# Kernel optimization log

Hardware: AMD Instinct MI355X
Metric: run time of the kernel (lower is better)

The kernel has to match this reference:

```python
import jax, jax.numpy as jnp
import numpy as np

U10_IDX, V10_IDX = 0, 1
WIND_THRESH = 0.5


def _gru(x, h, Wih, Whh, bih, bhh):
    # standard torch GRUCell math
    gi = x @ Wih.T + bih
    gh = h @ Whh.T + bhh
    ir, iz, inn = jnp.split(gi, 3, axis=-1)
    hr, hz, hnn = jnp.split(gh, 3, axis=-1)
    r = jax.nn.sigmoid(ir + hr)
    z = jax.nn.sigmoid(iz + hz)
    n = jnp.tanh(inn + r * hnn)
    return (1.0 - z) * n + z * h


def setup_inputs() -> dict:
    B, N, H, F, Th, Tf = 256, 184, 128, 8, 24, 24
    key = jax.random.key(0)
    ks = jax.random.split(key, 24)
    s = 0.1
    f32 = jnp.float32
    feature = jax.random.normal(ks[0], (B, Th + Tf, N, F), f32)
    pm25_hist = jax.random.uniform(ks[1], (B, Th, N, 1), dtype=f32)
    adj_mat = (jax.random.uniform(ks[2], (N, N)) < 0.1).astype(f32)
    angles = jax.random.uniform(ks[3], (N, N), f32, 0.0, 2.0 * np.pi)
    C = F + 1  # ChebConv in-channels = in_dim + out_dim
    return dict(
        feature=feature, pm25_hist=pm25_hist, adj_mat=adj_mat, angles=angles,
        W_ih_hist=s * jax.random.normal(ks[4], (3 * H, 2), f32),
        W_hh_hist=s * jax.random.normal(ks[5], (3 * H, H), f32),
        b_ih_hist=s * jax.random.normal(ks[6], (3 * H,), f32),
        b_hh_hist=s * jax.random.normal(ks[7], (3 * H,), f32),
        fc_hist_w=s * jax.random.normal(ks[8], (1, H), f32),
        fc_hist_b=s * jax.random.normal(ks[9], (1,), f32),
        cheb_w0=s * jax.random.normal(ks[10], (C, 1), f32),
        cheb_w1=s * jax.random.normal(ks[11], (C, 1), f32),
        cheb_b=s * jax.random.normal(ks[12], (1,), f32),
        W_ih=s * jax.random.normal(ks[13], (3 * H, C + 1), f32),
        W_hh=s * jax.random.normal(ks[14], (3 * H, H), f32),
        b_ih=s * jax.random.normal(ks[15], (3 * H,), f32),
        b_hh=s * jax.random.normal(ks[16], (3 * H,), f32),
        fc_out_w=s * jax.random.normal(ks[17], (1, H), f32),
        fc_out_b=s * jax.random.normal(ks[18], (1,), f32),
    )


def reference(feature, pm25_hist, adj_mat, angles,
              W_ih_hist, W_hh_hist, b_ih_hist, b_hh_hist,
              fc_hist_w, fc_hist_b,
              cheb_w0, cheb_w1, cheb_b,
              W_ih, W_hh, b_ih, b_hh,
              fc_out_w, fc_out_b):
    B, T, N, F = feature.shape
    H = W_hh.shape[1]
    Th = pm25_hist.shape[1]
    comp1 = jnp.cos(angles)                                # [N,N]
    comp2 = jnp.cos(angles - jnp.float32(np.pi / 2.0))     # [N,N]
    adj_b = adj_mat > 0

    # ---- history GRU over pm25_hist ----
    def hist_step(carry, p):
        hn, xn = carry
        x = jnp.concatenate([xn, p], axis=-1).reshape(B * N, 2)
        hn = _gru(x, hn, W_ih_hist, W_hh_hist, b_ih_hist, b_hh_hist)
        xn = hn.reshape(B, N, H) @ fc_hist_w.T + fc_hist_b
        return (hn, xn), None

    h0 = jnp.zeros((B * N, H), feature.dtype)
    x0 = jnp.zeros((B, N, 1), feature.dtype)
    (hn, xn), _ = jax.lax.scan(hist_step, (h0, x0), jnp.swapaxes(pm25_hist, 0, 1))

    # ---- forecast: dynamic wind-gated graph + ChebConv(K=2) + GRU ----
    def fore_step(carry, f):
        hn, xn = carry
        x = jnp.concatenate([xn, f], axis=-1)              # [B,N,F+1]
        u = f[..., U10_IDX]                                # [B,N]
        v = f[..., V10_IDX]
        wind = u[:, :, None] * comp1[None] + v[:, :, None] * comp2[None]
        # edge i->j iff adj and wind projection >= threshold
        M = jnp.logical_and(wind >= WIND_THRESH, adj_b[None]).astype(x.dtype)
        deg = M.sum(-1)                                    # source degree [B,N]
        has = deg > 0
        dinv = jnp.where(has, 1.0 / jnp.sqrt(jnp.where(has, deg, 1.0)), 0.0)
        # ChebConv scaled Laplacian (lambda_max=2, sym norm):
        # L_hat x [j] = -dinv_j * sum_i dinv_i * M[i,j] * x[i] + (0 if deg_j>0 else -1) * x[j]
        y = jnp.einsum('bij,bic->bjc', M * dinv[:, :, None], x)
        y = -dinv[:, :, None] * y + jnp.where(has, 0.0, -1.0)[:, :, None] * x
        g = jax.nn.sigmoid(x @ cheb_w0 + y @ cheb_w1 + cheb_b)  # [B,N,1]
        x2 = jnp.concatenate([x, g], axis=-1).reshape(B * N, F + 2)
        hn = _gru(x2, hn, W_ih, W_hh, b_ih, b_hh)
        xn = hn.reshape(B, N, H) @ fc_out_w.T + fc_out_b
        return (hn, xn), xn

    fore_feat = jnp.swapaxes(feature[:, Th:], 0, 1)        # [Tf,B,N,F]
    (_, _), preds = jax.lax.scan(fore_step, (hn, xn), fore_feat)
    return jnp.swapaxes(preds, 0, 1)                       # [B,Tf,N,1]
```

## Files before the change

### kernel.cpp

```cpp
#include <hip/hip_runtime.h>
#include <hip/hip_bf16.h>
#include <math.h>

#define BB 256
#define NN 184
#define HH 128
#define FF 8
#define TH 24
#define TF 24
#define KA 160
#define NG2 640
#define RPAD 192
#define STRH 136
#define NT 1024
#define NW3 552
#define LOG2E 1.44269504088896f

#define REC_F 8832
#define OFF_DINV 4416
#define OFF_G 5152
#define OFF_AXF 5888

typedef __attribute__((ext_vector_type(8))) short bf16x8;
typedef __attribute__((ext_vector_type(4))) short bf16x4;
typedef __attribute__((ext_vector_type(4))) float f32x4;
typedef __attribute__((ext_vector_type(2))) unsigned u32x2;

#if __has_builtin(__builtin_amdgcn_mfma_f32_16x16x16bf16_1k)
#define XK16 1
#else
#define XK16 0
#endif

#if __has_builtin(__builtin_amdgcn_exp2f)
#define EXP2(x) __builtin_amdgcn_exp2f(x)
#else
#define EXP2(x) exp2f(x)
#endif

__device__ __forceinline__ unsigned short f2bf(float f) {
    unsigned u = __float_as_uint(f);
    u += 0x7fffu + ((u >> 16) & 1u);
    return (unsigned short)(u >> 16);
}
__device__ __forceinline__ unsigned pkbf(float a, float b) {
    __hip_bfloat162 h = __float22bfloat162_rn(make_float2(a, b));
    return *reinterpret_cast<unsigned*>(&h);
}
__device__ __forceinline__ void gload16(const void* src, void* dst) {
    __builtin_amdgcn_global_load_lds(
        (const __attribute__((address_space(1))) unsigned int*)src,
        (__attribute__((address_space(3))) unsigned int*)dst, 16, 0, 0);
}

__global__ void prep_weights(const float* __restrict__ WhhH, const float* __restrict__ WihH,
                             const float* __restrict__ WhhF, const float* __restrict__ WihF,
                             const float* __restrict__ bihH, const float* __restrict__ bhhH,
                             const float* __restrict__ bihF, const float* __restrict__ bhhF,
                             const float* __restrict__ fchw, const float* __restrict__ fchb,
                             unsigned short* __restrict__ WaH, unsigned short* __restrict__ WaF) {
    int idx = blockIdx.x * 256 + threadIdx.x;
    if (idx >= NG2 * KA) return;
    int jp = idx / KA, k = idx % KA;
    int j = jp & 127, part = jp >> 7;
    float vh = 0.f, vf = 0.f;
    if (part <= 1) {
        int row = part * 128 + j;
        if (k < 128) {
            vh = WhhH[row * 128 + k] + WihH[row * 2 + 0] * fchw[k];
            vf = WhhF[row * 128 + k];
        } else {
            int s = k - 128;
            if (s == 0)  vh = WihH[row * 2 + 1];
            if (s < 8)   vf = WihF[row * 10 + (s + 1)];
            if (s == 8)  { vh = WihH[row * 2 + 0]; vf = WihF[row * 10 + 0]; }
            if (s == 9)  vf = WihF[row * 10 + 9];
            if (s == 11) {
                vh = bihH[row] + bhhH[row] + WihH[row * 2 + 0] * fchb[0];
                vf = bihF[row] + bhhF[row];
            }
        }
    } else if (part == 2) {
        if (k < 128) { vh = WhhH[(256 + j) * 128 + k]; vf = WhhF[(256 + j) * 128 + k]; }
        else if (k == 139) { vh = bhhH[256 + j]; vf = bhhF[256 + j]; }
    } else if (part == 3) {
        if (k >= 128) {
            int s = k - 128;
            if (s == 0)  vh = WihH[(256 + j) * 2 + 1];
            if (s < 8)   vf = WihF[(256 + j) * 10 + (s + 1)];
            if (s == 8)  { vh = WihH[(256 + j) * 2 + 0]; vf = WihF[(256 + j) * 10 + 0]; }
            if (s == 9)  vf = WihF[(256 + j) * 10 + 9];
            if (s == 11) {
                vh = bihH[256 + j] + WihH[(256 + j) * 2 + 0] * fchb[0];
                vf = bihF[256 + j];
            }
        }
    } else {
        if (k < 128) vh = WihH[(256 + j) * 2 + 0] * fchw[k];
    }
    float sc = (part <= 1) ? LOG2E : 2.0f * LOG2E;
    WaH[idx] = f2bf(vh * sc);
    WaF[idx] = f2bf(vf * sc);
}

__global__ void prep_edges(const float* __restrict__ angles, const float* __restrict__ adj,
                           float4* __restrict__ edges, int* __restrict__ cnt) {
    int idx = blockIdx.x * 256 + threadIdx.x;
    if (idx < NN * NN && adj[idx] > 0.f) {
        float a = angles[idx];
        int pos = atomicAdd(cnt, 1);
        float4 r;
        r.x = cosf(a);
        r.y = cosf(a - 1.57079632679489662f);
        r.z = __int_as_float(idx / NN);
        r.w = __int_as_float(idx % NN);
        edges[pos] = r;
    }
}

__global__ __launch_bounds__(256) void prep_graph(
    const float* __restrict__ feature, const float* __restrict__ pm25,
    const float4* __restrict__ edges, const int* __restrict__ ecnt,
    const float* __restrict__ cw0, const float* __restrict__ cw1,
    const float* __restrict__ cbb, char* __restrict__ xrec,
    unsigned short* __restrict__ phist)
{
    const int bt = blockIdx.x;
    const int b = bt / (TH + TF), tt = bt % (TH + TF);
    const int tid = threadIdx.x;

    if (tt < TH) {
        if (tid < NN)
            phist[(long)b * (TH * NN) + tt * NN + tid] =
                f2bf(pm25[((long)b * TH + tt) * NN + tid]);
        return;
    }

    char* rec = xrec + ((long)b * TF + (tt - TH)) * REC_F;

    __shared__ float f8[NN * FF];
    __shared__ unsigned long long mT[NN][3];
    __shared__ int dg[NN];
    __shared__ float di[NN];
    __shared__ float red[NW3][8];

    const float4* fb4 = (const float4*)(feature + ((long)b * (TH + TF) + tt) * (NN * FF));
    for (int i = tid; i < (NN * FF) / 4; i += 256) ((float4*)f8)[i] = fb4[i];
    for (int i = tid; i < NN * 3; i += 256) ((unsigned long long*)mT)[i] = 0ull;
    for (int i = tid; i < NN; i += 256) dg[i] = 0;
    __syncthreads();
    const int nE = *ecnt;
    for (int e = tid; e < nE; e += 256) {
        float4 r = edges[e];
        int ii = __float_as_int(r.z), jj = __float_as_int(r.w);
        if (f8[ii * FF] * r.x + f8[ii * FF + 1] * r.y >= 0.5f) {
            atomicAdd(&dg[ii], 1);
            atomicOr(&mT[jj][ii >> 6], 1ull << (ii & 63));
        }
    }
    __syncthreads();
    if (tid < NN) di[tid] = (dg[tid] > 0) ? rsqrtf((float)dg[tid]) : 0.f;
    __syncthreads();
    unsigned long long* mr = (unsigned long long*)rec;
    for (int i = tid; i < NW3; i += 256) mr[i] = ((const unsigned long long*)mT)[i];
    for (int task = tid; task < NW3; task += 256) {
        int j = task / 3, wd = task - j * 3;
        unsigned long long m = mT[j][wd];
        float acc[8];
        #pragma unroll
        for (int c = 0; c < 8; ++c) acc[c] = 0.f;
        while (m) {
            int bp = __ffsll(m) - 1; m &= m - 1;
            int i = wd * 64 + bp;
            float d = di[i];
            #pragma unroll
            for (int c = 0; c < 8; ++c) acc[c] += d * f8[i * FF + c];
        }
        #pragma unroll
        for (int c = 0; c < 8; ++c) red[task][c] = acc[c];
    }
    __syncthreads();
    if (tid < NN) {
        int j = tid;
        float dj = di[j];
        float hzj = (dj > 0.f) ? 0.f : -1.f;
        float G = cbb[0];
        #pragma unroll
        for (int c = 0; c < 8; ++c) {
            float accc = red[j * 3 + 0][c] + red[j * 3 + 1][c] + red[j * 3 + 2][c];
            float xv = f8[j * FF + c];
            float y = -dj * accc + hzj * xv;
            G += xv * cw0[c + 1] + y * cw1[c + 1];
        }
        ((float*)(rec + OFF_DINV))[j] = dj;
        ((float*)(rec + OFF_G))[j] = G;
        unsigned short* ax = (unsigned short*)(rec + OFF_AXF) + j * 8;
        #pragma unroll
        for (int c = 0; c < 8; ++c) ax[c] = f2bf(f8[j * FF + c]);
    }
}

__global__ __launch_bounds__(NT, 4) void fused_dgc(
    const unsigned short* __restrict__ WaH,
    const unsigned short* __restrict__ WaF,
    const float* __restrict__ fchw, const float* __restrict__ fchb,
    const float* __restrict__ fcow, const float* __restrict__ fcob,
    const float* __restrict__ cw0, const float* __restrict__ cw1,
    const char* __restrict__ xrec, const unsigned short* __restrict__ phist,
    float* __restrict__ pred)
{
    __shared__ unsigned short Ah[2][RPAD * STRH];
    __shared__ unsigned short AxR[RPAD * 8];
    __shared__ __align__(16) char stg[2][8960];
    __shared__ float red_s[RPAD * 9];
    __shared__ float2 dx_s[NN];
    __shared__ float fcls_f[132];
    __shared__ unsigned short zero16[8];
    __shared__ __align__(16) unsigned short phist_s[TH * NN + 16];

    const int tid = threadIdx.x;
    const int bb = blockIdx.x;
    const int w = tid >> 6, lane = tid & 63, q = lane >> 4, lq = lane & 15;
    const int cg = w & 7, rh = w >> 3;

    for (int i = tid; i < RPAD * STRH; i += NT) Ah[0][i] = 0;
    for (int i = tid; i < RPAD * 8; i += NT)
        AxR[i] = ((i & 7) == 3) ? (unsigned short)0x3F80 : (unsigned short)0;
    if (tid < 8) zero16[tid] = 0;
    if (tid < NN) dx_s[tid] = make_float2(0.f, 0.f);

    bf16x8 wregH[4][4];
#if XK16
    bf16x4 wregX[4];
#else
    bf16x8 wregX[4];
#endif
    auto load_w = [&](const unsigned short* Wa, const float* fcw, const float* fcb, bool h4) {
        const int jcol = cg * 16 + lq;
        #pragma unroll
        for (int g = 0; g < 3; ++g)
            #pragma unroll
            for (int kc = 0; kc < 4; ++kc)
                wregH[g][kc] = *(const bf16x8*)(Wa + (long)(g * 128 + jcol) * KA + kc * 32 + q * 8);
        if (h4)
            #pragma unroll
            for (int kc = 0; kc < 4; ++kc)
                wregH[3][kc] = *(const bf16x8*)(Wa + (long)(4 * 128 + jcol) * KA + kc * 32 + q * 8);
        #pragma unroll
        for (int g = 0; g < 4; ++g)
#if XK16
            wregX[g] = *(const bf16x4*)(Wa + (long)(g * 128 + jcol) * KA + 128 + q * 4);
#else
            wregX[g] = *(const bf16x8*)(Wa + (long)(g * 128 + jcol) * KA + 128 + q * 8);
#endif
        if (tid < 132) fcls_f[tid] = (tid < 128) ? fcw[tid] : ((tid == 128) ? fcb[0] : 0.f);
    };
    load_w(WaH, fchw, fchb, true);

    if (tid < NW3)
        gload16((const char*)phist + (long)bb * (TH * NN * 2) + tid * 16,
                (char*)phist_s + (tid & ~63) * 16);

    const float w00 = cw0[0], w10 = cw1[0];
    const float fcbH = fchb[0];

    int p = 0;
    __syncthreads();

    for (int t = 0; t < TH + TF; ++t) {
        const bool hist = (t < TH);
        const bool dofc = (t >= TH - 1);
        const unsigned short* AxFS = (const unsigned short*)(stg[p] + OFF_AXF);

        if (!hist) {
            const unsigned long long* maskS = (const unsigned long long*)stg[p];
            const float* GS = (const float*)(stg[p] + OFF_G);
            const int jg = tid >> 2, wd = tid & 3;
            if (jg < NN) {
                unsigned long long m = (wd < 3) ? maskS[jg * 3 + wd] : 0ull;
                float acc = 0.f;
                while (m) {
                    int bp = __ffsll(m) - 1; m &= m - 1;
                    float2 dxv = dx_s[wd * 64 + bp];
                    acc += dxv.x * dxv.y;
                }
                acc += __shfl_xor(acc, 1);
                acc += __shfl_xor(acc, 2);
                if (wd == 0) {
                    float2 dxj = dx_s[jg];
                    float hzj = (dxj.x > 0.f) ? 0.f : -1.f;
                    float y0 = -dxj.x * acc + hzj * dxj.y;
                    float pre = GS[jg] + dxj.y * w00 + y0 * w10;
                    float g = __builtin_amdgcn_rcpf(1.0f + EXP2(-LOG2E * pre));
                    AxR[jg * 8 + 1] = f2bf(g);
                }
            }
            __syncthreads();
        }

        const int t2 = t + 1;
        if (t2 >= TH && t2 < TH + TF && tid < NW3)
            gload16(xrec + ((long)bb * TF + (t2 - TH)) * REC_F + tid * 16,
                    (char*)stg[p ^ 1] + (tid & ~63) * 16);

        f32x4 fw = *(const f32x4*)&fcls_f[cg * 16 + q * 4];
        const unsigned short corr0 = (t == 0) ? f2bf(-fcbH) : (unsigned short)0;
        #pragma unroll
        for (int rl = 0; rl < 6; ++rl) {
            const int row = rh * 96 + rl * 16 + lq;
            const int ro = row * STRH;
            f32x4 a0 = {0.f,0.f,0.f,0.f}, a1 = {0.f,0.f,0.f,0.f}, a2 = {0.f,0.f,0.f,0.f};
            f32x4 a3 = {0.f,0.f,0.f,0.f};
            #pragma unroll
            for (int kc = 0; kc < 4; ++kc) {
                bf16x8 bh = *(const bf16x8*)(&Ah[p][ro + kc * 32 + q * 8]);
                a0 = __builtin_amdgcn_mfma_f32_16x16x32_bf16(wregH[0][kc], bh, a0, 0, 0, 0);
                a1 = __builtin_amdgcn_mfma_f32_16x16x32_bf16(wregH[1][kc], bh, a1, 0, 0, 0);
                a2 = __builtin_amdgcn_mfma_f32_16x16x32_bf16(wregH[2][kc], bh, a2, 0, 0, 0);
                if (hist)
                    a3 = __builtin_amdgcn_mfma_f32_16x16x32_bf16(wregH[3][kc], bh, a3, 0, 0, 0);
            }
#if XK16
            bf16x4 bx;
            if (hist) {
                unsigned short pb = phist_s[t * NN + row];
                bf16x4 z = {0,0,0,0};
                bx = z;
                if (q == 0) bx[0] = (short)pb;
                if (q == 2) { bx[0] = (short)corr0; bx[3] = (short)0x3F80; }
            } else {
                const unsigned short* bxp = (q < 2) ? (AxFS + row * 8 + q * 4)
                                          : (q == 2) ? (AxR + row * 8) : zero16;
                bx = *(const bf16x4*)bxp;
            }
            a0 = __builtin_amdgcn_mfma_f32_16x16x16bf16_1k(wregX[0], bx, a0, 0, 0, 0);
            a1 = __builtin_amdgcn_mfma_f32_16x16x16bf16_1k(wregX[1], bx, a1, 0, 0, 0);
            a2 = __builtin_amdgcn_mfma_f32_16x16x16bf16_1k(wregX[2], bx, a2, 0, 0, 0);
            a3 = __builtin_amdgcn_mfma_f32_16x16x16bf16_1k(wregX[3], bx, a3, 0, 0, 0);
#else
            bf16x8 bx;
            if (hist) {
                unsigned short pb = phist_s[t * NN + row];
                bf16x8 z = {0,0,0,0,0,0,0,0};
                bx = z;
                if (q == 0) bx[0] = (short)pb;
                if (q == 1) { bx[0] = (short)corr0; bx[3] = (short)0x3F80; }
            } else {
                const unsigned short* bxp = (q == 0) ? (AxFS + row * 8)
                                          : (q == 1) ? (AxR + row * 8) : zero16;
                bx = *(const bf16x8*)bxp;
            }
            a0 = __builtin_amdgcn_mfma_f32_16x16x32_bf16(wregX[0], bx, a0, 0, 0, 0);
            a1 = __builtin_amdgcn_mfma_f32_16x16x32_bf16(wregX[1], bx, a1, 0, 0, 0);
            a2 = __builtin_amdgcn_mfma_f32_16x16x32_bf16(wregX[2], bx, a2, 0, 0, 0);
            a3 = __builtin_amdgcn_mfma_f32_16x16x32_bf16(wregX[3], bx, a3, 0, 0, 0);
#endif

            u32x2 hold = *(const u32x2*)&Ah[p][ro + cg * 16 + q * 4];

            float hn[4];
            #pragma unroll
            for (int rg = 0; rg < 4; ++rg) {
                unsigned hu = hold[rg >> 1];
                float ho = ((rg & 1) == 0) ? __uint_as_float(hu << 16)
                                           : __uint_as_float(hu & 0xffff0000u);
                float rr = __builtin_amdgcn_rcpf(1.0f + EXP2(-a0[rg]));
                float zz = __builtin_amdgcn_rcpf(1.0f + EXP2(-a1[rg]));
                float wv = fmaf(rr, a2[rg], a3[rg]);
                unsigned sg = __float_as_uint(wv) & 0x80000000u;
                float e = EXP2(-fabsf(wv));
                float tv = (1.0f - e) * __builtin_amdgcn_rcpf(1.0f + e);
                tv = __uint_as_float(__float_as_uint(tv) ^ sg);
                hn[rg] = fmaf(zz, ho - tv, tv);
            }
            u32x2 pk;
            pk[0] = pkbf(hn[0], hn[1]);
            pk[1] = pkbf(hn[2], hn[3]);
            *(u32x2*)&Ah[p ^ 1][ro + cg * 16 + q * 4] = pk;
            if (dofc) {
                float pf = hn[0] * fw.x + hn[1] * fw.y + hn[2] * fw.z + hn[3] * fw.w;
                pf += __shfl_xor(pf, 16);
                pf += __shfl_xor(pf, 32);
                if (q == 0) red_s[row * 9 + cg] = pf;
            }
        }
        __syncthreads();

        if (dofc) {
            if (tid < NN) {
                float xn = fcls_f[128];
                #pragma unroll
                for (int c = 0; c < 8; ++c) xn += red_s[tid * 9 + c];
                float dv = 0.f;
                if (t2 >= TH && t2 < TH + TF)
                    dv = *(const float*)(stg[p ^ 1] + OFF_DINV + tid * 4);
                dx_s[tid] = make_float2(dv, xn);
                AxR[tid * 8 + 0] = f2bf(xn);
                if (t >= TH) pred[((long)bb * TF + (t - TH)) * NN + tid] = xn;
            }
            __syncthreads();
        }

        if (t == TH - 1)
            load_w(WaF, fcow, fcob, false);
        p ^= 1;
    }
}

extern "C" void kernel_launch(void* const* d_in, const int* in_sizes, int n_in,
                              void* d_out, int out_size, void* d_ws, size_t ws_size,
                              hipStream_t stream) {
    const float* feature = (const float*)d_in[0];
    const float* pm25    = (const float*)d_in[1];
    const float* adj     = (const float*)d_in[2];
    const float* angles  = (const float*)d_in[3];
    const float* W_ih_h  = (const float*)d_in[4];
    const float* W_hh_h  = (const float*)d_in[5];
    const float* b_ih_h  = (const float*)d_in[6];
    const float* b_hh_h  = (const float*)d_in[7];
    const float* fch_w   = (const float*)d_in[8];
    const float* fch_b   = (const float*)d_in[9];
    const float* cw0     = (const float*)d_in[10];
    const float* cw1     = (const float*)d_in[11];
    const float* cbb     = (const float*)d_in[12];
    const float* W_ih    = (const float*)d_in[13];
    const float* W_hh    = (const float*)d_in[14];
    const float* b_ih    = (const float*)d_in[15];
    const float* b_hh    = (const float*)d_in[16];
    const float* fco_w   = (const float*)d_in[17];
    const float* fco_b   = (const float*)d_in[18];
    float* pred = (float*)d_out;

    char* ws = (char*)d_ws;
    size_t off = 0;
    unsigned short* WaH   = (unsigned short*)(ws + off); off += (size_t)NG2 * KA * 2;
    unsigned short* WaF   = (unsigned short*)(ws + off); off += (size_t)NG2 * KA * 2;
    float4*         edges = (float4*)(ws + off);         off += (size_t)NN * NN * 16;
    int*            cnt   = (int*)(ws + off);            off += 16;
    unsigned short* phist = (unsigned short*)(ws + off); off += (size_t)BB * TH * NN * 2;
    char*           xrec  = (char*)(ws + off);
    off += (size_t)BB * TF * REC_F;

    hipMemsetAsync(cnt, 0, 16, stream);
    prep_weights<<<(NG2 * KA + 255) / 256, 256, 0, stream>>>(
        W_hh_h, W_ih_h, W_hh, W_ih, b_ih_h, b_hh_h, b_ih, b_hh, fch_w, fch_b,
        WaH, WaF);
    prep_edges<<<(NN * NN + 255) / 256, 256, 0, stream>>>(angles, adj, edges, cnt);
    prep_graph<<<BB * (TH + TF), 256, 0, stream>>>(
        feature, pm25, edges, cnt, cw0, cw1, cbb, xrec, phist);

    fused_dgc<<<BB, NT, 0, stream>>>(
        WaH, WaF, fch_w, fch_b, fco_w, fco_b, cw0, cw1, xrec, phist, pred);
}
```

Baseline: 645.0 us.

## Fold fc-output reduction into graph step via shared atomics, drop extra barrier

The per-row fc output is now accumulated with shared-memory atomics into a double-buffered xnraw array instead of a red_s buffer followed by a separate reduction pass and barrier. The bias add, the bf16 write into AxR, the prediction store and the dinv lookup move into the next step's graph-convolution phase, which removes one __syncthreads per timestep. The history pm25 conversion is split into its own small elementwise kernel, so prep_graph launches only forecast blocks. Shared atomics add contention (8 adds per row), and the bias for the first forecast step is handled as a special case.

```diff
diff --git a/kernel.cpp b/kernel.cpp
--- a/kernel.cpp
+++ b/kernel.cpp
@@ -118,25 +118,23 @@
     }
 }
 
+__global__ void prep_hist(const float* __restrict__ pm25, unsigned short* __restrict__ phist) {
+    int idx = blockIdx.x * 256 + threadIdx.x;
+    if (idx < BB * TH * NN) phist[idx] = f2bf(pm25[idx]);
+}
+
 __global__ __launch_bounds__(256) void prep_graph(
-    const float* __restrict__ feature, const float* __restrict__ pm25,
+    const float* __restrict__ feature,
     const float4* __restrict__ edges, const int* __restrict__ ecnt,
     const float* __restrict__ cw0, const float* __restrict__ cw1,
-    const float* __restrict__ cbb, char* __restrict__ xrec,
-    unsigned short* __restrict__ phist)
+    const float* __restrict__ cbb, char* __restrict__ xrec)
 {
     const int bt = blockIdx.x;
-    const int b = bt / (TH + TF), tt = bt % (TH + TF);
+    const int b = bt / TF, tf = bt % TF;
+    const int tt = TH + tf;
     const int tid = threadIdx.x;
 
-    if (tt < TH) {
-        if (tid < NN)
-            phist[(long)b * (TH * NN) + tt * NN + tid] =
-                f2bf(pm25[((long)b * TH + tt) * NN + tid]);
-        return;
-    }
-
-    char* rec = xrec + ((long)b * TF + (tt - TH)) * REC_F;
+    char* rec = xrec + ((long)b * TF + tf) * REC_F;
 
     __shared__ float f8[NN * FF];
     __shared__ unsigned long long mT[NN][3];
@@ -212,8 +210,7 @@
     __shared__ unsigned short Ah[2][RPAD * STRH];
     __shared__ unsigned short AxR[RPAD * 8];
     __shared__ __align__(16) char stg[2][8960];
-    __shared__ float red_s[RPAD * 9];
-    __shared__ float2 dx_s[NN];
+    __shared__ float xnraw[2][RPAD];
     __shared__ float fcls_f[132];
     __shared__ unsigned short zero16[8];
     __shared__ __align__(16) unsigned short phist_s[TH * NN + 16];
@@ -227,7 +224,7 @@
     for (int i = tid; i < RPAD * 8; i += NT)
         AxR[i] = ((i & 7) == 3) ? (unsigned short)0x3F80 : (unsigned short)0;
     if (tid < 8) zero16[tid] = 0;
-    if (tid < NN) dx_s[tid] = make_float2(0.f, 0.f);
+    if (tid < RPAD) { xnraw[0][tid] = 0.f; xnraw[1][tid] = 0.f; }
 
     bf16x8 wregH[4][4];
 #if XK16
@@ -262,7 +259,7 @@
                 (char*)phist_s + (tid & ~63) * 16);
 
     const float w00 = cw0[0], w10 = cw1[0];
-    const float fcbH = fchb[0];
+    const float fcbH = fchb[0], fcbO = fcob[0];
 
     int p = 0;
     __syncthreads();
@@ -274,26 +271,40 @@
 
         if (!hist) {
             const unsigned long long* maskS = (const unsigned long long*)stg[p];
+            const float* dinS = (const float*)(stg[p] + OFF_DINV);
             const float* GS = (const float*)(stg[p] + OFF_G);
+            const float* xr = xnraw[(t - 1) & 1];
+            const float fcbP = (t == TH) ? fcbH : fcbO;
             const int jg = tid >> 2, wd = tid & 3;
             if (jg < NN) {
-                unsigned long long m = (wd < 3) ? maskS[jg * 3 + wd] : 0ull;
-                float acc = 0.f;
-                while (m) {
-                    int bp = __ffsll(m) - 1; m &= m - 1;
-                    float2 dxv = dx_s[wd * 64 + bp];
-                    acc += dxv.x * dxv.y;
+                float acc = 0.f, accd = 0.f;
+                if (wd < 3) {
+                    unsigned long long m = maskS[jg * 3 + wd];
+                    while (m) {
+                        int bp = __ffsll(m) - 1; m &= m - 1;
+                        int i = wd * 64 + bp;
+                        float d = dinS[i];
+                        acc = fmaf(d, xr[i], acc);
+                        accd += d;
+                    }
                 }
-                acc += __shfl_xor(acc, 1);
-                acc += __shfl_xor(acc, 2);
+                acc  += __shfl_xor(acc, 1);  acc  += __shfl_xor(acc, 2);
+                accd += __shfl_xor(accd, 1); accd += __shfl_xor(accd, 2);
                 if (wd == 0) {
-                    float2 dxj = dx_s[jg];
-                    float hzj = (dxj.x > 0.f) ? 0.f : -1.f;
-                    float y0 = -dxj.x * acc + hzj * dxj.y;
-                    float pre = GS[jg] + dxj.y * w00 + y0 * w10;
+                    float dj = dinS[jg];
+                    float xnj = xr[jg] + fcbP;
+                    float hzj = (dj > 0.f) ? 0.f : -1.f;
+                    float sum = fmaf(fcbP, accd, acc);
+                    float y0 = -dj * sum + hzj * xnj;
+                    float pre = GS[jg] + xnj * w00 + y0 * w10;
                     float g = __builtin_amdgcn_rcpf(1.0f + EXP2(-LOG2E * pre));
                     AxR[jg * 8 + 1] = f2bf(g);
+                    AxR[jg * 8 + 0] = f2bf(xnj);
+                    if (t > TH) pred[((long)bb * TF + (t - 1 - TH)) * NN + jg] = xnj;
                 }
+            } else {
+                int i = tid - 736;
+                if (i < RPAD) xnraw[t & 1][i] = 0.f;
             }
             __syncthreads();
         }
@@ -381,30 +392,19 @@
                 float pf = hn[0] * fw.x + hn[1] * fw.y + hn[2] * fw.z + hn[3] * fw.w;
                 pf += __shfl_xor(pf, 16);
                 pf += __shfl_xor(pf, 32);
-                if (q == 0) red_s[row * 9 + cg] = pf;
+                if (q == 0) atomicAdd(&xnraw[t & 1][row], pf);
             }
         }
         __syncthreads();
-
-        if (dofc) {
-            if (tid < NN) {
-                float xn = fcls_f[128];
-                #pragma unroll
-                for (int c = 0; c < 8; ++c) xn += red_s[tid * 9 + c];
-                float dv = 0.f;
-                if (t2 >= TH && t2 < TH + TF)
-                    dv = *(const float*)(stg[p ^ 1] + OFF_DINV + tid * 4);
-                dx_s[tid] = make_float2(dv, xn);
-                AxR[tid * 8 + 0] = f2bf(xn);
-                if (t >= TH) pred[((long)bb * TF + (t - TH)) * NN + tid] = xn;
-            }
-            __syncthreads();
-        }
 
         if (t == TH - 1)
             load_w(WaF, fcow, fcob, false);
         p ^= 1;
     }
+
+    if (tid < NN)
+        pred[((long)bb * TF + (TF - 1)) * NN + tid] =
+            xnraw[(TH + TF - 1) & 1][tid] + fcbO;
 }
 
 extern "C" void kernel_launch(void* const* d_in, const int* in_sizes, int n_in,
@@ -446,8 +446,9 @@
         W_hh_h, W_ih_h, W_hh, W_ih, b_ih_h, b_hh_h, b_ih, b_hh, fch_w, fch_b,
         WaH, WaF);
     prep_edges<<<(NN * NN + 255) / 256, 256, 0, stream>>>(angles, adj, edges, cnt);
-    prep_graph<<<BB * (TH + TF), 256, 0, stream>>>(
-        feature, pm25, edges, cnt, cw0, cw1, cbb, xrec, phist);
+    prep_hist<<<(BB * TH * NN + 255) / 256, 256, 0, stream>>>(pm25, phist);
+    prep_graph<<<BB * TF, 256, 0, stream>>>(
+        feature, edges, cnt, cw0, cw1, cbb, xrec);
 
     fused_dgc<<<BB, NT, 0, stream>>>(
         WaH, WaF, fch_w, fch_b, fco_w, fco_b, cw0, cw1, xrec, phist, pred);
```

After: 619.3 us. 1.04x faster.
